# Performance work log

Hardware: AMD Instinct MI355X
Metric: run time of the kernel (lower is better)

## Reference

```python
import jax, jax.numpy as jnp
import numpy as np

WIN = 8
HEADS = 8
DOWN = 4
STRIDE = WIN // DOWN  # 2
LEVELS = len([i for i in range(8) if WIN / DOWN**i >= 1])  # 2
EPS = 1e-5


def circular_pad(x, pad_r, pad_b):
    # x: (N, H, W, C) -> (N, H+pad_b, W+pad_r, C), circular repeat like torch repeat+slice
    N, H, W, C = x.shape
    Hr = -(-(H + pad_b) // H)
    Wr = -(-(W + pad_r) // W)
    return jnp.tile(x, (1, Hr, Wr, 1))[:, :H + pad_b, :W + pad_r, :]


def pad_fit_win(x, ws):
    N, H, W, C = x.shape
    H_ = -(-H // ws) * ws
    W_ = -(-W // ws) * ws
    return circular_pad(x, W_ - W, H_ - H)


def window_partition(x, ws):
    N, H, W, C = x.shape
    x = x.reshape(N, H // ws, ws, W // ws, ws, C)
    return x.transpose(0, 1, 3, 2, 4, 5).reshape(-1, ws, ws, C)


def window_reverse(w, ws, H, W):
    B = w.shape[0] // ((H // ws) * (W // ws))
    x = w.reshape(B, H // ws, W // ws, ws, ws, -1)
    return x.transpose(0, 1, 3, 2, 4, 5).reshape(B, H, W, -1)


def layernorm(x, g, b):
    mu = jnp.mean(x, -1, keepdims=True)
    var = jnp.var(x, -1, keepdims=True)
    return (x - mu) * jax.lax.rsqrt(var + EPS) * g + b


def mha(q, k, v, wq, wk, wv, wf, bf):
    # q: (B, Lq, C); k, v: (B, Lk, C). Weights stored as (in, out); eval mode (no dropout).
    B, Lq, C = q.shape
    Lk = k.shape[1]
    dh = C // HEADS
    qh = (q @ wq).reshape(B, Lq, HEADS, dh)
    kh = (k @ wk).reshape(B, Lk, HEADS, dh)
    vh = (v @ wv).reshape(B, Lk, HEADS, dh)
    attn = jnp.einsum('bqhd,bkhd->bhqk', qh, kh) * (1.0 / dh ** 0.5)
    attn = jax.nn.softmax(attn, axis=-1)
    o = jnp.einsum('bhqk,bkhd->bqhd', attn, vh).reshape(B, Lq, C)
    return o @ wf + bf


def self_attention(x, wq, wk, wv, wf, bf):
    N, H, W, C = x.shape
    xp = pad_fit_win(x, WIN)
    _, H_, W_, _ = xp.shape
    xw = window_partition(xp, WIN).reshape(-1, WIN * WIN, C)
    res = mha(xw, xw, xw, wq, wk, wv, wf, bf)
    res = window_reverse(res.reshape(-1, WIN, WIN, C), WIN, H_, W_)
    return (xp + res)[:, :H, :W, :]


def cross_attention(q, kv, wq, wk, wv, wf, bf):
    # q: (N,qH,qW,C) non-overlapping windows; kv: (N,kH,kW,C) overlapping unfold windows
    N, qH, qW, C = q.shape
    _, kH, kW, _ = kv.shape
    qp = pad_fit_win(q, WIN)
    _, qH_, qW_, _ = qp.shape
    qw = window_partition(qp, WIN).reshape(-1, WIN * WIN, C)
    kH_ = (-(-kH // STRIDE) - 1) * STRIDE + WIN
    kW_ = (-(-kW // STRIDE) - 1) * STRIDE + WIN
    kvp = circular_pad(kv, kW_ - kW, kH_ - kH)
    nH = (kH_ - WIN) // STRIDE + 1
    nW = (kW_ - WIN) // STRIDE + 1
    ri = (jnp.arange(nH) * STRIDE)[:, None] + jnp.arange(WIN)
    ci = (jnp.arange(nW) * STRIDE)[:, None] + jnp.arange(WIN)
    patches = kvp[:, ri][:, :, :, ci]
    patches = patches.transpose(0, 1, 3, 2, 4, 5).reshape(-1, WIN * WIN, C)
    res = mha(qw, patches, patches, wq, wk, wv, wf, bf)
    res = window_reverse(res.reshape(-1, WIN, WIN, C), WIN, qH_, qW_)
    return (qp + res)[:, :qH, :qW, :]


def avgpool4(x):  # NHWC avg pool with kernel=stride=DOWN
    N, H, W, C = x.shape
    return x.reshape(N, H // DOWN, DOWN, W // DOWN, DOWN, C).mean((2, 4))


def setup_inputs() -> dict:
    key = jax.random.key(0)
    ks = jax.random.split(key, 12)
    D, DF = 256, 1024
    N, H, W = 8, 128, 128
    s = 0.02

    def w(k, shape):
        return jax.random.normal(k, shape, jnp.float32) * s

    return {
        'x': jax.random.normal(ks[0], (N, D, H, W), jnp.float32),
        'sa_wq': w(ks[1], (D, D)), 'sa_wk': w(ks[2], (D, D)), 'sa_wv': w(ks[3], (D, D)),
        'sa_wf': w(ks[4], (D, D)), 'sa_bf': jnp.zeros((D,), jnp.float32),
        'ca_wq': w(ks[5], (D, D)), 'ca_wk': w(ks[6], (D, D)), 'ca_wv': w(ks[7], (D, D)),
        'ca_wf': w(ks[8], (D, D)), 'ca_bf': jnp.zeros((D,), jnp.float32),
        'ln_self_g': jnp.ones((D,), jnp.float32), 'ln_self_b': jnp.zeros((D,), jnp.float32),
        'ln_cross_g': jnp.ones((D,), jnp.float32), 'ln_cross_b': jnp.zeros((D,), jnp.float32),
        'ffn_w1': w(ks[9], (D, DF)), 'ffn_b1': jnp.zeros((DF,), jnp.float32),
        'ffn_w2': w(ks[10], (DF, D)), 'ffn_b2': jnp.zeros((D,), jnp.float32),
        'ln_out_g': jnp.ones((D,), jnp.float32), 'ln_out_b': jnp.zeros((D,), jnp.float32),
    }


def reference(x, sa_wq, sa_wk, sa_wv, sa_wf, sa_bf,
              ca_wq, ca_wk, ca_wv, ca_wf, ca_bf,
              ln_self_g, ln_self_b, ln_cross_g, ln_cross_b,
              ffn_w1, ffn_b1, ffn_w2, ffn_b2, ln_out_g, ln_out_b):
    N, C, H, W = x.shape
    xh = x.transpose(0, 2, 3, 1)  # NHWC
    xh = pad_fit_win(xh, WIN)
    attn_list = []
    for idx in range(LEVELS):
        xa = self_attention(xh, sa_wq, sa_wk, sa_wv, sa_wf, sa_bf)
        xa = layernorm(xa, ln_self_g, ln_self_b)
        attn_list.append(xa)
        if idx < LEVELS - 1:
            xh = avgpool4(xa)
    kv = attn_list[-1]
    for idx in range(LEVELS - 1, 0, -1):
        q = cross_attention(attn_list[idx - 1], kv, ca_wq, ca_wk, ca_wv, ca_wf, ca_bf)
        q = layernorm(q, ln_cross_g, ln_cross_b)
        kv = q
    q = kv[:, :H, :W, :]
    res = jax.nn.relu(q @ ffn_w1 + ffn_b1) @ ffn_w2 + ffn_b2
    out = layernorm(q + res, ln_out_g, ln_out_b)
    return out.transpose(0, 3, 1, 2)
```

## Files before the change

### kernel.cpp

```cpp
#include <hip/hip_runtime.h>

typedef _Float16 h16;
typedef _Float16 f16x8 __attribute__((ext_vector_type(8)));
typedef _Float16 f16x4 __attribute__((ext_vector_type(4)));
typedef float f32x4 __attribute__((ext_vector_type(4)));

__device__ __forceinline__ float b2f(h16 v){ return (float)v; }
__device__ __forceinline__ h16 f2b(float v){ return (h16)v; }

#define CDIM 256
#define NHEADS 8
#define DH 32

__global__ __launch_bounds__(256) void k_wt_all(const float* __restrict__ s0, const float* __restrict__ s1,
                                                const float* __restrict__ s2, const float* __restrict__ s3,
                                                const float* __restrict__ s4, const float* __restrict__ s5,
                                                const float* __restrict__ s6, const float* __restrict__ s7,
                                                const float* __restrict__ s8, const float* __restrict__ s9,
                                                h16* __restrict__ wsc)
{
    __shared__ float T[32][33];
    int b = blockIdx.x;
    const float* src; h16* dst; int K, N, ti, tj;
    if (b < 512) {
        int w = b >> 6, rem = b & 63;
        ti = rem >> 3; tj = rem & 7; K = 256; N = 256;
        switch (w) {
            case 0: src = s0; break; case 1: src = s1; break;
            case 2: src = s2; break; case 3: src = s3; break;
            case 4: src = s4; break; case 5: src = s5; break;
            case 6: src = s6; break; default: src = s7; break;
        }
        dst = wsc + w * 65536;
    } else if (b < 768) {
        int rem = b - 512; ti = rem >> 5; tj = rem & 31; K = 256; N = 1024;
        src = s8; dst = wsc + 8 * 65536;
    } else {
        int rem = b - 768; ti = rem >> 3; tj = rem & 7; K = 1024; N = 256;
        src = s9; dst = wsc + 8 * 65536 + 262144;
    }
    int rr = threadIdx.x >> 5, c = threadIdx.x & 31;
    #pragma unroll
    for (int i = 0; i < 4; ++i) {
        int r = i * 8 + rr;
        T[r][c] = src[(long long)(ti * 32 + r) * N + tj * 32 + c];
    }
    __syncthreads();
    #pragma unroll
    for (int i = 0; i < 4; ++i) {
        int r = i * 8 + rr;
        dst[(long long)(tj * 32 + r) * K + ti * 32 + c] = f2b(T[c][r]);
    }
}

__global__ __launch_bounds__(256) void k_nchw2nhwc(const float* __restrict__ x, h16* __restrict__ o,
                                                   int Hh, int Ww)
{
    __shared__ float T[64][65];
    int bid = blockIdx.x;
    int cb = bid & 3; bid >>= 2;
    int nwb = Ww >> 6;
    int wb = bid % nwb; bid /= nwb;
    int h = bid % Hh;
    int n = bid / Hh;
    int lane = threadIdx.x & 63, grp = threadIdx.x >> 6;
    int w0 = wb << 6;
    long long HW = (long long)Hh * Ww;
    long long rbase = ((long long)(n * CDIM + cb * 64) * Hh + h) * Ww + w0;
    #pragma unroll
    for (int i = 0; i < 16; ++i) {
        int cl = grp * 16 + i;
        T[cl][lane] = x[rbase + (long long)cl * HW + lane];
    }
    __syncthreads();
    long long obase = (long long)(n * Hh + h) * Ww + w0;
    #pragma unroll
    for (int i = 0; i < 16; ++i) {
        int wl = grp * 16 + i;
        o[(obase + wl) * CDIM + cb * 64 + lane] = f2b(T[lane][wl]);
    }
}

__global__ __launch_bounds__(256) void k_gemm_mfma(const h16* __restrict__ A, const h16* __restrict__ Bt,
                                                   const float* __restrict__ bias, const h16* __restrict__ Cadd,
                                                   h16* __restrict__ C,
                                                   int N, int K, int ldA, int ldbt, int ldc,
                                                   long long ostride, int relu)
{
    __shared__ __align__(16) h16 As[128 * 64];
    __shared__ __align__(16) h16 Bs[128 * 64];
    const int tid = threadIdx.x;
    const int wave = tid >> 6, lane = tid & 63;
    const int l15 = lane & 15, g = lane >> 4;
    const int gx = gridDim.x;
    int L = blockIdx.y * gx + blockIdx.x;
    const int nwg = gx * gridDim.y;
    if ((nwg & 7) == 0) {
        const int cpx = nwg >> 3;
        L = (L & 7) * cpx + (L >> 3);
    }
    const int row0 = (L / gx) * 128, col0 = (L % gx) * 128;
    const int wm = (wave >> 1) * 64, wn = (wave & 1) * 64;

    f32x4 acc[4][4] = {};

    const int srow = wave * 32 + (lane >> 3);
    const int sch  = ((lane & 7) ^ (srow & 7)) * 8;
    const h16* ag = A  + (long long)(row0 + srow) * ldA  + sch;
    const h16* bg = Bt + (long long)(col0 + srow) * ldbt + sch;
    h16* as_base = As + (wave * 32) * 64;
    h16* bs_base = Bs + (wave * 32) * 64;

    for (int k0 = 0; k0 < K; k0 += 64) {
        #pragma unroll
        for (int i = 0; i < 4; ++i) {
            __builtin_amdgcn_global_load_lds(
                (const __attribute__((address_space(1))) void*)(ag + (long long)i * 8 * ldA),
                (__attribute__((address_space(3))) void*)(as_base + i * 8 * 64), 16, 0, 0);
            __builtin_amdgcn_global_load_lds(
                (const __attribute__((address_space(1))) void*)(bg + (long long)i * 8 * ldbt),
                (__attribute__((address_space(3))) void*)(bs_base + i * 8 * 64), 16, 0, 0);
        }
        ag += 64; bg += 64;
        __syncthreads();
        #pragma unroll
        for (int kk = 0; kk < 2; ++kk) {
            const int c = kk * 4 + g;
            const int slot = (c ^ (l15 & 7)) << 3;
            f16x8 af[4], bb[4];
            #pragma unroll
            for (int i = 0; i < 4; ++i) {
                af[i] = *(const f16x8*)(As + (wm + i * 16 + l15) * 64 + slot);
                bb[i] = *(const f16x8*)(Bs + (wn + i * 16 + l15) * 64 + slot);
            }
            #pragma unroll
            for (int i = 0; i < 4; ++i)
                #pragma unroll
                for (int j = 0; j < 4; ++j)
                    acc[i][j] = __builtin_amdgcn_mfma_f32_16x16x32_f16(af[i], bb[j], acc[i][j], 0, 0, 0);
        }
        __syncthreads();
    }

    const int cr = g * 4;
    #pragma unroll
    for (int j = 0; j < 4; ++j) {
        int col = col0 + wn + j * 16 + l15;
        int grp = col >> 8;
        long long cb = (long long)grp * ostride + (col & 255);
        float bv = bias ? bias[col] : 0.f;
        #pragma unroll
        for (int i = 0; i < 4; ++i) {
            #pragma unroll
            for (int r = 0; r < 4; ++r) {
                long long row = row0 + wm + i * 16 + cr + r;
                float v = acc[i][j][r] + bv;
                if (relu) v = fmaxf(v, 0.f);
                long long addr = cb + row * ldc;
                if (Cadd) v += b2f(Cadd[addr]);
                C[addr] = f2b(v);
            }
        }
    }
}

__global__ __launch_bounds__(512) void k_gemm_ln(const h16* __restrict__ A, const h16* __restrict__ Bt,
                                                 const float* __restrict__ bias, const h16* __restrict__ Cadd,
                                                 const h16* __restrict__ R,
                                                 const float* __restrict__ gw, const float* __restrict__ bw,
                                                 h16* __restrict__ O16, float* __restrict__ O32,
                                                 int K, int ldA, int ldbt, int HW, int mode)
{
    __shared__ __align__(16) h16 As[128 * 64];
    __shared__ __align__(16) h16 Bs[256 * 64];
    __shared__ float red[2][128][4];
    const int tid = threadIdx.x;
    const int wave = tid >> 6, lane = tid & 63;
    const int l15 = lane & 15, g = lane >> 4;
    const int row0 = blockIdx.x * 128;
    const int wm = (wave >> 2) * 64, wn = (wave & 3) * 64;

    f32x4 acc[4][4] = {};

    const int ar = wave * 16 + (lane >> 3);
    const int br = wave * 32 + (lane >> 3);
    const int ach = ((lane & 7) ^ (ar & 7)) * 8;
    const int bch = ((lane & 7) ^ (br & 7)) * 8;
    const h16* ag = A  + (long long)(row0 + ar) * ldA + ach;
    const h16* bg = Bt + (long long)br * ldbt + bch;
    h16* as_base = As + (wave * 16) * 64;
    h16* bs_base = Bs + (wave * 32) * 64;

    for (int k0 = 0; k0 < K; k0 += 64) {
        #pragma unroll
        for (int i = 0; i < 2; ++i)
            __builtin_amdgcn_global_load_lds(
                (const __attribute__((address_space(1))) void*)(ag + (long long)i * 8 * ldA),
                (__attribute__((address_space(3))) void*)(as_base + i * 8 * 64), 16, 0, 0);
        #pragma unroll
        for (int i = 0; i < 4; ++i)
            __builtin_amdgcn_global_load_lds(
                (const __attribute__((address_space(1))) void*)(bg + (long long)i * 8 * ldbt),
                (__attribute__((address_space(3))) void*)(bs_base + i * 8 * 64), 16, 0, 0);
        ag += 64; bg += 64;
        __syncthreads();
        #pragma unroll
        for (int kk = 0; kk < 2; ++kk) {
            const int c = kk * 4 + g;
            const int slot = (c ^ (l15 & 7)) << 3;
            f16x8 af[4], bb[4];
            #pragma unroll
            for (int i = 0; i < 4; ++i) {
                af[i] = *(const f16x8*)(As + (wm + i * 16 + l15) * 64 + slot);
                bb[i] = *(const f16x8*)(Bs + (wn + i * 16 + l15) * 64 + slot);
            }
            #pragma unroll
            for (int i = 0; i < 4; ++i)
                #pragma unroll
                for (int j = 0; j < 4; ++j)
                    acc[i][j] = __builtin_amdgcn_mfma_f32_16x16x32_f16(af[i], bb[j], acc[i][j], 0, 0, 0);
        }
        __syncthreads();
    }

    float sr[4][4] = {}, sr2[4][4] = {};
    #pragma unroll
    for (int j = 0; j < 4; ++j) {
        int col = wn + j * 16 + l15;
        float bv = bias ? bias[col] : 0.f;
        #pragma unroll
        for (int i = 0; i < 4; ++i) {
            #pragma unroll
            for (int r = 0; r < 4; ++r) {
                long long row = row0 + wm + i * 16 + g * 4 + r;
                float u = acc[i][j][r] + bv;
                if (Cadd) u += b2f(Cadd[row * CDIM + col]);
                u += b2f(R[row * CDIM + col]);
                acc[i][j][r] = u;
                sr[i][r] += u; sr2[i][r] += u * u;
            }
        }
    }
    #pragma unroll
    for (int i = 0; i < 4; ++i)
        #pragma unroll
        for (int r = 0; r < 4; ++r) {
            float s = sr[i][r], s2 = sr2[i][r];
            #pragma unroll
            for (int off = 1; off < 16; off <<= 1) { s += __shfl_xor(s, off); s2 += __shfl_xor(s2, off); }
            sr[i][r] = s; sr2[i][r] = s2;
        }
    if (l15 == 0) {
        #pragma unroll
        for (int i = 0; i < 4; ++i)
            #pragma unroll
            for (int r = 0; r < 4; ++r) {
                int lr = wm + i * 16 + g * 4 + r;
                red[0][lr][wave & 3] = sr[i][r];
                red[1][lr][wave & 3] = sr2[i][r];
            }
    }
    __syncthreads();
    float mu_[4][4], iv_[4][4];
    #pragma unroll
    for (int i = 0; i < 4; ++i)
        #pragma unroll
        for (int r = 0; r < 4; ++r) {
            int lr = wm + i * 16 + g * 4 + r;
            f32x4 p = *(const f32x4*)&red[0][lr][0];
            f32x4 q = *(const f32x4*)&red[1][lr][0];
            float ts  = p[0] + p[1] + p[2] + p[3];
            float ts2 = q[0] + q[1] + q[2] + q[3];
            float mu = ts * (1.f / 256.f);
            mu_[i][r] = mu;
            iv_[i][r] = rsqrtf(ts2 * (1.f / 256.f) - mu * mu + 1e-5f);
        }
    if (mode == 0) {
        #pragma unroll
        for (int j = 0; j < 4; ++j) {
            int col = wn + j * 16 + l15;
            float gc = gw[col], bc = bw[col];
            #pragma unroll
            for (int i = 0; i < 4; ++i)
                #pragma unroll
                for (int r = 0; r < 4; ++r) {
                    long long row = row0 + wm + i * 16 + g * 4 + r;
                    O16[row * CDIM + col] = f2b((acc[i][j][r] - mu_[i][r]) * iv_[i][r] * gc + bc);
                }
        }
    } else {
        #pragma unroll
        for (int j = 0; j < 4; ++j) {
            int col = wn + j * 16 + l15;
            float gc = gw[col], bc = bw[col];
            #pragma unroll
            for (int i = 0; i < 4; ++i) {
                int tok0 = row0 + wm + i * 16 + g * 4;
                int n = tok0 / HW, hw = tok0 - n * HW;
                f32x4 y;
                #pragma unroll
                for (int r = 0; r < 4; ++r)
                    y[r] = (acc[i][j][r] - mu_[i][r]) * iv_[i][r] * gc + bc;
                *(f32x4*)(O32 + (long long)(n * CDIM + col) * HW + hw) = y;
            }
        }
    }
}

__global__ __launch_bounds__(256) void k_attn_mfma(const h16* __restrict__ Q, const h16* __restrict__ Kp,
                                                   const h16* __restrict__ Vp, h16* __restrict__ O,
                                                   int Hh, int Ww, int cross)
{
    __shared__ __align__(16) h16 SpA[4][64 * 64];
    __shared__ __align__(16) h16 VtA[4][32 * 64];
    const int tid = threadIdx.x;
    const int wave = tid >> 6, lane = tid & 63;
    const int l15 = lane & 15, g = lane >> 4;
    h16* Sp = SpA[wave];
    h16* Vt = VtA[wave];

    const int win = blockIdx.x;
    int n, wi, wj;
    if (cross) { n = win >> 8; wi = (win >> 4) & 15; wj = win & 15; }
    else {
        int nw = Ww >> 3, nh = Hh >> 3;
        n = win / (nh * nw);
        int rem = win - n * (nh * nw);
        wi = rem / nw; wj = rem - (rem / nw) * nw;
    }
    auto qtok = [&](int t) {
        return cross ? (n * 128 + wi * 8 + (t >> 3)) * 128 + wj * 8 + (t & 7)
                     : (n * Hh + wi * 8 + (t >> 3)) * Ww + wj * 8 + (t & 7);
    };
    auto ktok = [&](int t) {
        return cross ? (n * 32 + ((wi * 2 + (t >> 3)) & 31)) * 32 + ((wj * 2 + (t & 7)) & 31)
                     : qtok(t);
    };
    const float scale = 0.17677669529663687f;

    int qt_frag[4], kt_frag[4];
    #pragma unroll
    for (int i = 0; i < 4; ++i) { qt_frag[i] = qtok(i * 16 + l15); kt_frag[i] = ktok(i * 16 + l15); }
    const int vtok = ktok(lane);
    int otok[4][4];
    #pragma unroll
    for (int qt = 0; qt < 4; ++qt)
        #pragma unroll
        for (int rr = 0; rr < 4; ++rr)
            otok[qt][rr] = qtok(qt * 16 + g * 4 + rr);

    #pragma unroll 1
    for (int hh = 0; hh < 2; ++hh) {
        const int h = wave * 2 + hh;
        const int hoff = h * 32;

        f16x8 vin[4];
        #pragma unroll
        for (int j = 0; j < 4; ++j)
            vin[j] = *(const f16x8*)(Vp + (long long)vtok * CDIM + hoff + j * 8);

        f16x8 kf[4], qf[4];
        #pragma unroll
        for (int i = 0; i < 4; ++i) {
            kf[i] = *(const f16x8*)(Kp + (long long)kt_frag[i] * CDIM + hoff + g * 8);
            qf[i] = *(const f16x8*)(Q  + (long long)qt_frag[i] * CDIM + hoff + g * 8);
        }

        #pragma unroll
        for (int j = 0; j < 4; ++j)
            #pragma unroll
            for (int e = 0; e < 8; ++e) {
                int d = j * 8 + e;
                Vt[(d * 64 + lane) ^ ((d & 7) << 3)] = vin[j][e];
            }

        f32x4 sT[4][4] = {};
        #pragma unroll
        for (int i = 0; i < 4; ++i)
            #pragma unroll
            for (int jq = 0; jq < 4; ++jq)
                sT[i][jq] = __builtin_amdgcn_mfma_f32_16x16x32_f16(kf[i], qf[jq], sT[i][jq], 0, 0, 0);

        #pragma unroll
        for (int jq = 0; jq < 4; ++jq) {
            float m = -1e30f;
            #pragma unroll
            for (int i = 0; i < 4; ++i)
                #pragma unroll
                for (int rr = 0; rr < 4; ++rr)
                    m = fmaxf(m, sT[i][jq][rr]);
            m = fmaxf(m, __shfl_xor(m, 16));
            m = fmaxf(m, __shfl_xor(m, 32));
            float p[16];
            float sum = 0.f;
            #pragma unroll
            for (int i = 0; i < 4; ++i)
                #pragma unroll
                for (int rr = 0; rr < 4; ++rr) {
                    float e = __expf((sT[i][jq][rr] - m) * scale);
                    p[i * 4 + rr] = e; sum += e;
                }
            sum += __shfl_xor(sum, 16);
            sum += __shfl_xor(sum, 32);
            float inv = 1.f / sum;
            int q = jq * 16 + l15;
            int rowbase = q * 64, swz = (q & 7) << 3;
            #pragma unroll
            for (int i = 0; i < 4; ++i) {
                f16x4 pk;
                pk[0] = (h16)(p[i * 4 + 0] * inv);
                pk[1] = (h16)(p[i * 4 + 1] * inv);
                pk[2] = (h16)(p[i * 4 + 2] * inv);
                pk[3] = (h16)(p[i * 4 + 3] * inv);
                *(f16x4*)(Sp + ((rowbase + i * 16 + g * 4) ^ swz)) = pk;
            }
        }
        asm volatile("s_waitcnt lgkmcnt(0)" ::: "memory");

        f32x4 o[4][2] = {};
        #pragma unroll
        for (int kb = 0; kb < 2; ++kb) {
            f16x8 vb[2];
            #pragma unroll
            for (int dt = 0; dt < 2; ++dt) {
                int d = dt * 16 + l15;
                vb[dt] = *(const f16x8*)(Vt + ((d * 64 + kb * 32 + g * 8) ^ ((d & 7) << 3)));
            }
            #pragma unroll
            for (int qt = 0; qt < 4; ++qt) {
                int q = qt * 16 + l15;
                f16x8 pa = *(const f16x8*)(Sp + ((q * 64 + kb * 32 + g * 8) ^ ((q & 7) << 3)));
                #pragma unroll
                for (int dt = 0; dt < 2; ++dt)
                    o[qt][dt] = __builtin_amdgcn_mfma_f32_16x16x32_f16(pa, vb[dt], o[qt][dt], 0, 0, 0);
            }
        }

        #pragma unroll
        for (int qt = 0; qt < 4; ++qt)
            #pragma unroll
            for (int rr = 0; rr < 4; ++rr) {
                long long tb = (long long)otok[qt][rr] * CDIM + hoff;
                #pragma unroll
                for (int dt = 0; dt < 2; ++dt)
                    O[tb + dt * 16 + l15] = f2b(o[qt][dt][rr]);
            }
        asm volatile("s_waitcnt lgkmcnt(0)" ::: "memory");
    }
}

__global__ __launch_bounds__(256) void k_ln_out(const h16* __restrict__ A, const h16* __restrict__ Bb,
                                                const float* __restrict__ g, const float* __restrict__ be,
                                                float* __restrict__ O, int HW)
{
    __shared__ float Y[32][257];
    int tid = threadIdx.x;
    int t = tid >> 5;
    int j = tid & 31;
    long long tok0 = (long long)blockIdx.x * 32;
    f32x4 g0 = *(const f32x4*)(g + j * 8),  g1 = *(const f32x4*)(g + j * 8 + 4);
    f32x4 e0 = *(const f32x4*)(be + j * 8), e1 = *(const f32x4*)(be + j * 8 + 4);
    #pragma unroll
    for (int pass = 0; pass < 4; ++pass) {
        int ta = pass * 8 + t;
        long long base = (tok0 + ta) * CDIM + j * 8;
        f16x8 a = *(const f16x8*)(A + base);
        f16x8 b = *(const f16x8*)(Bb + base);
        float v[8]; float s = 0.f, s2 = 0.f;
        #pragma unroll
        for (int e = 0; e < 8; ++e) { float vv = b2f(a[e]) + b2f(b[e]); v[e] = vv; s += vv; s2 += vv * vv; }
        #pragma unroll
        for (int off = 1; off < 32; off <<= 1) { s += __shfl_xor(s, off); s2 += __shfl_xor(s2, off); }
        float mu = s * (1.f / 256.f);
        float inv = rsqrtf(s2 * (1.f / 256.f) - mu * mu + 1e-5f);
        #pragma unroll
        for (int e = 0; e < 4; ++e) Y[ta][j * 8 + e]     = (v[e] - mu) * inv * g0[e] + e0[e];
        #pragma unroll
        for (int e = 0; e < 4; ++e) Y[ta][j * 8 + 4 + e] = (v[e + 4] - mu) * inv * g1[e] + e1[e];
    }
    __syncthreads();
    int n = (int)(tok0 / HW);
    int hw0 = (int)(tok0 - (long long)n * HW);
    int tt = tid & 31;
    int cw = tid >> 5;
    #pragma unroll
    for (int k = 0; k < 32; ++k) {
        int c = k * 8 + cw;
        O[((long long)(n * CDIM + c)) * HW + hw0 + tt] = Y[tt][c];
    }
}

__global__ __launch_bounds__(256) void k_pool(const h16* __restrict__ A, h16* __restrict__ P,
                                              int Hin, int Win)
{
    int tok = blockIdx.x, c = threadIdx.x;
    int Wo = Win >> 2, Ho = Hin >> 2;
    int n = tok / (Ho * Wo);
    int rem = tok - n * (Ho * Wo);
    int i = rem / Wo, j = rem - (rem / Wo) * Wo;
    float s = 0.f;
    #pragma unroll
    for (int di = 0; di < 4; ++di)
        #pragma unroll
        for (int dj = 0; dj < 4; ++dj)
            s += b2f(A[(((long long)n * Hin + i * 4 + di) * Win + j * 4 + dj) * CDIM + c]);
    P[(long long)tok * CDIM + c] = f2b(s * 0.0625f);
}

extern "C" void kernel_launch(void* const* d_in, const int* in_sizes, int n_in,
                              void* d_out, int out_size, void* d_ws, size_t ws_size,
                              hipStream_t stream)
{
    const float* x     = (const float*)d_in[0];
    const float* sa_wq = (const float*)d_in[1];
    const float* sa_wk = (const float*)d_in[2];
    const float* sa_wv = (const float*)d_in[3];
    const float* sa_wf = (const float*)d_in[4];
    const float* sa_bf = (const float*)d_in[5];
    const float* ca_wq = (const float*)d_in[6];
    const float* ca_wk = (const float*)d_in[7];
    const float* ca_wv = (const float*)d_in[8];
    const float* ca_wf = (const float*)d_in[9];
    const float* ca_bf = (const float*)d_in[10];
    const float* lns_g = (const float*)d_in[11];
    const float* lns_b = (const float*)d_in[12];
    const float* lnc_g = (const float*)d_in[13];
    const float* lnc_b = (const float*)d_in[14];
    const float* w1    = (const float*)d_in[15];
    const float* b1    = (const float*)d_in[16];
    const float* w2    = (const float*)d_in[17];
    const float* b2    = (const float*)d_in[18];
    const float* lno_g = (const float*)d_in[19];
    const float* lno_b = (const float*)d_in[20];
    float* out = (float*)d_out;

    const int TOK0 = 8 * 128 * 128;
    const int TOK1 = 8 * 32 * 32;
    const size_t S0  = (size_t)TOK0 * CDIM * sizeof(h16);
    const size_t SML = (size_t)TOK1 * CDIM * sizeof(h16);
    char* ws = (char*)d_ws;
    h16* W0 = (h16*)(ws);
    h16* W1 = (h16*)(ws + S0);
    h16* W2 = (h16*)(ws + 2 * S0);
    h16* W3 = (h16*)(ws + 3 * S0);
    h16* H  = W2;
    h16* P1 = (h16*)(ws + 0 * SML);
    h16* Q1 = (h16*)(ws + 1 * SML);
    h16* K1 = (h16*)(ws + 2 * SML);
    h16* V1 = (h16*)(ws + 3 * SML);
    h16* A1 = (h16*)(ws + 5 * SML);
    h16* Kc = (h16*)(ws + 6 * SML);
    h16* Vc = (h16*)(ws + 7 * SML);

    const size_t WSC_BYTES = (8 * 65536 + 262144 + 262144) * sizeof(h16);
    bool tailws = ws_size >= 4 * S0 + WSC_BYTES;
    h16* wsc = tailws ? (h16*)(ws + 4 * S0) : (h16*)d_out;
    h16* sa_wqT = wsc + 0 * 65536;
    h16* sa_wfT = wsc + 3 * 65536;
    h16* ca_wqT = wsc + 4 * 65536;
    h16* ca_wkT = wsc + 5 * 65536;
    h16* ca_wfT = wsc + 7 * 65536;
    h16* w1T    = wsc + 8 * 65536;
    h16* w2T    = wsc + 8 * 65536 + 262144;

    const long long OS0 = (long long)TOK0 * CDIM;
    const long long OS1 = (long long)TOK1 * CDIM;

    dim3 blk(256), blk2(512);

    k_wt_all<<<1024, blk, 0, stream>>>(sa_wq, sa_wk, sa_wv, sa_wf, ca_wq, ca_wk, ca_wv, ca_wf,
                                       w1, w2, wsc);

    k_nchw2nhwc<<<8 * 128 * 2 * 4, blk, 0, stream>>>(x, W0, 128, 128);
    k_gemm_mfma<<<dim3(6, TOK0 / 128), blk, 0, stream>>>(W0, sa_wqT, nullptr, nullptr, W1, 768, 256, 256, 256, 256, OS0, 0);
    k_attn_mfma<<<TOK0 / 64, blk, 0, stream>>>(W1, W2, W3, W1, 128, 128, 0);
    k_gemm_ln<<<TOK0 / 128, blk2, 0, stream>>>(W1, sa_wfT, sa_bf, nullptr, W0, lns_g, lns_b,
                                               W3, nullptr, 256, 256, 256, 16384, 0);

    k_pool<<<TOK1, blk, 0, stream>>>(W3, P1, 128, 128);
    k_gemm_mfma<<<dim3(6, TOK1 / 128), blk, 0, stream>>>(P1, sa_wqT, nullptr, nullptr, Q1, 768, 256, 256, 256, 256, OS1, 0);
    k_attn_mfma<<<TOK1 / 64, blk, 0, stream>>>(Q1, K1, V1, Q1, 32, 32, 0);
    k_gemm_ln<<<TOK1 / 128, blk2, 0, stream>>>(Q1, sa_wfT, sa_bf, nullptr, P1, lns_g, lns_b,
                                               A1, nullptr, 256, 256, 256, 1024, 0);

    k_gemm_mfma<<<dim3(2, TOK0 / 128), blk, 0, stream>>>(W3, ca_wqT, nullptr, nullptr, W1, 256, 256, 256, 256, 256, 0, 0);
    k_gemm_mfma<<<dim3(4, TOK1 / 128), blk, 0, stream>>>(A1, ca_wkT, nullptr, nullptr, Kc, 512, 256, 256, 256, 256, OS1, 0);
    k_attn_mfma<<<TOK0 / 64, blk, 0, stream>>>(W1, Kc, Vc, W1, 0, 0, 1);
    k_gemm_ln<<<TOK0 / 128, blk2, 0, stream>>>(W1, ca_wfT, ca_bf, nullptr, W3, lnc_g, lnc_b,
                                               W1, nullptr, 256, 256, 256, 16384, 0);

    k_gemm_mfma<<<dim3(4, TOK0 / 128), blk, 0, stream>>>(W1, w1T,             b1,       nullptr, H,  512, 256, 256, 256, 512, 256, 1);
    k_gemm_mfma<<<dim3(2, TOK0 / 128), blk, 0, stream>>>(H,  w2T,             b2,       nullptr, W0, 256, 512, 512, 1024, 256, 0, 0);
    k_gemm_mfma<<<dim3(4, TOK0 / 128), blk, 0, stream>>>(W1, w1T + 512 * 256, b1 + 512, nullptr, H,  512, 256, 256, 256, 512, 256, 1);
    if (tailws) {
        k_gemm_ln<<<TOK0 / 128, blk2, 0, stream>>>(H, w2T + 512, nullptr, W0, W1, lno_g, lno_b,
                                                   nullptr, out, 512, 512, 1024, 16384, 1);
    } else {
        k_gemm_mfma<<<dim3(2, TOK0 / 128), blk, 0, stream>>>(H, w2T + 512, nullptr, W0, W0, 256, 512, 512, 1024, 256, 0, 0);
        k_ln_out<<<TOK0 / 32, blk, 0, stream>>>(W1, W0, lno_g, lno_b, out, 16384);
    }
}
```

Baseline: 1.156 ms.

## Double-buffer LDS tiles in MFMA GEMM kernels to overlap loads with compute

Both GEMM kernels now use two LDS buffers per operand. The next K tile is issued with async global-to-LDS loads before the current tile is computed, and partial vmcnt waits replace the full __syncthreads. The goal is to hide global memory latency behind the MFMA work. The cost is twice the LDS use, which may lower occupancy, especially in the LN kernel with its 256-wide B tile. Ordering now relies on hand-set vmcnt counts, which must match the number of loads issued per stage.

```diff
diff --git a/kernel.cpp b/kernel.cpp
--- a/kernel.cpp
+++ b/kernel.cpp
@@ -87,8 +87,8 @@
                                                    int N, int K, int ldA, int ldbt, int ldc,
                                                    long long ostride, int relu)
 {
-    __shared__ __align__(16) h16 As[128 * 64];
-    __shared__ __align__(16) h16 Bs[128 * 64];
+    __shared__ __align__(16) h16 As[2 * 128 * 64];
+    __shared__ __align__(16) h16 Bs[2 * 128 * 64];
     const int tid = threadIdx.x;
     const int wave = tid >> 6, lane = tid & 63;
     const int l15 = lane & 15, g = lane >> 4;
@@ -111,18 +111,35 @@
     h16* as_base = As + (wave * 32) * 64;
     h16* bs_base = Bs + (wave * 32) * 64;
 
-    for (int k0 = 0; k0 < K; k0 += 64) {
+    const int NT = K >> 6;
+    auto stage = [&](int t, int buf) {
+        const h16* a = ag + (long long)t * 64;
+        const h16* b = bg + (long long)t * 64;
+        h16* ad = as_base + buf * (128 * 64);
+        h16* bd = bs_base + buf * (128 * 64);
         #pragma unroll
         for (int i = 0; i < 4; ++i) {
             __builtin_amdgcn_global_load_lds(
-                (const __attribute__((address_space(1))) void*)(ag + (long long)i * 8 * ldA),
-                (__attribute__((address_space(3))) void*)(as_base + i * 8 * 64), 16, 0, 0);
+                (const __attribute__((address_space(1))) void*)(a + (long long)i * 8 * ldA),
+                (__attribute__((address_space(3))) void*)(ad + i * 8 * 64), 16, 0, 0);
             __builtin_amdgcn_global_load_lds(
-                (const __attribute__((address_space(1))) void*)(bg + (long long)i * 8 * ldbt),
-                (__attribute__((address_space(3))) void*)(bs_base + i * 8 * 64), 16, 0, 0);
-        }
-        ag += 64; bg += 64;
-        __syncthreads();
+                (const __attribute__((address_space(1))) void*)(b + (long long)i * 8 * ldbt),
+                (__attribute__((address_space(3))) void*)(bd + i * 8 * 64), 16, 0, 0);
+        }
+    };
+
+    stage(0, 0);
+    int cur = 0;
+    for (int t = 0; t < NT; ++t) {
+        if (t + 1 < NT) {
+            stage(t + 1, cur ^ 1);
+            asm volatile("s_waitcnt vmcnt(8)" ::: "memory");
+        } else {
+            asm volatile("s_waitcnt vmcnt(0)" ::: "memory");
+        }
+        __builtin_amdgcn_s_barrier();
+        const h16* Ab = As + cur * (128 * 64);
+        const h16* Bb2 = Bs + cur * (128 * 64);
         #pragma unroll
         for (int kk = 0; kk < 2; ++kk) {
             const int c = kk * 4 + g;
@@ -130,8 +147,8 @@
             f16x8 af[4], bb[4];
             #pragma unroll
             for (int i = 0; i < 4; ++i) {
-                af[i] = *(const f16x8*)(As + (wm + i * 16 + l15) * 64 + slot);
-                bb[i] = *(const f16x8*)(Bs + (wn + i * 16 + l15) * 64 + slot);
+                af[i] = *(const f16x8*)(Ab + (wm + i * 16 + l15) * 64 + slot);
+                bb[i] = *(const f16x8*)(Bb2 + (wn + i * 16 + l15) * 64 + slot);
             }
             #pragma unroll
             for (int i = 0; i < 4; ++i)
@@ -139,10 +156,10 @@
                 for (int j = 0; j < 4; ++j)
                     acc[i][j] = __builtin_amdgcn_mfma_f32_16x16x32_f16(af[i], bb[j], acc[i][j], 0, 0, 0);
         }
-        __syncthreads();
-    }
-
-    const int cr = g * 4;
+        __builtin_amdgcn_s_barrier();
+        cur ^= 1;
+    }
+
     #pragma unroll
     for (int j = 0; j < 4; ++j) {
         int col = col0 + wn + j * 16 + l15;
@@ -153,7 +170,7 @@
         for (int i = 0; i < 4; ++i) {
             #pragma unroll
             for (int r = 0; r < 4; ++r) {
-                long long row = row0 + wm + i * 16 + cr + r;
+                long long row = row0 + wm + i * 16 + g * 4 + r;
                 float v = acc[i][j][r] + bv;
                 if (relu) v = fmaxf(v, 0.f);
                 long long addr = cb + row * ldc;
@@ -171,8 +188,8 @@
                                                  h16* __restrict__ O16, float* __restrict__ O32,
                                                  int K, int ldA, int ldbt, int HW, int mode)
 {
-    __shared__ __align__(16) h16 As[128 * 64];
-    __shared__ __align__(16) h16 Bs[256 * 64];
+    __shared__ __align__(16) h16 As[2 * 128 * 64];
+    __shared__ __align__(16) h16 Bs[2 * 256 * 64];
     __shared__ float red[2][128][4];
     const int tid = threadIdx.x;
     const int wave = tid >> 6, lane = tid & 63;
@@ -191,19 +208,36 @@
     h16* as_base = As + (wave * 16) * 64;
     h16* bs_base = Bs + (wave * 32) * 64;
 
-    for (int k0 = 0; k0 < K; k0 += 64) {
+    const int NT = K >> 6;
+    auto stage = [&](int t, int buf) {
+        const h16* a = ag + (long long)t * 64;
+        const h16* b = bg + (long long)t * 64;
+        h16* ad = as_base + buf * (128 * 64);
+        h16* bd = bs_base + buf * (256 * 64);
         #pragma unroll
         for (int i = 0; i < 2; ++i)
             __builtin_amdgcn_global_load_lds(
-                (const __attribute__((address_space(1))) void*)(ag + (long long)i * 8 * ldA),
-                (__attribute__((address_space(3))) void*)(as_base + i * 8 * 64), 16, 0, 0);
+                (const __attribute__((address_space(1))) void*)(a + (long long)i * 8 * ldA),
+                (__attribute__((address_space(3))) void*)(ad + i * 8 * 64), 16, 0, 0);
         #pragma unroll
         for (int i = 0; i < 4; ++i)
             __builtin_amdgcn_global_load_lds(
-                (const __attribute__((address_space(1))) void*)(bg + (long long)i * 8 * ldbt),
-                (__attribute__((address_space(3))) void*)(bs_base + i * 8 * 64), 16, 0, 0);
-        ag += 64; bg += 64;
-        __syncthreads();
+                (const __attribute__((address_space(1))) void*)(b + (long long)i * 8 * ldbt),
+                (__attribute__((address_space(3))) void*)(bd + i * 8 * 64), 16, 0, 0);
+    };
+
+    stage(0, 0);
+    int cur = 0;
+    for (int t = 0; t < NT; ++t) {
+        if (t + 1 < NT) {
+            stage(t + 1, cur ^ 1);
+            asm volatile("s_waitcnt vmcnt(6)" ::: "memory");
+        } else {
+            asm volatile("s_waitcnt vmcnt(0)" ::: "memory");
+        }
+        __builtin_amdgcn_s_barrier();
+        const h16* Ab = As + cur * (128 * 64);
+        const h16* Bb2 = Bs + cur * (256 * 64);
         #pragma unroll
         for (int kk = 0; kk < 2; ++kk) {
             const int c = kk * 4 + g;
@@ -211,8 +245,8 @@
             f16x8 af[4], bb[4];
             #pragma unroll
             for (int i = 0; i < 4; ++i) {
-                af[i] = *(const f16x8*)(As + (wm + i * 16 + l15) * 64 + slot);
-                bb[i] = *(const f16x8*)(Bs + (wn + i * 16 + l15) * 64 + slot);
+                af[i] = *(const f16x8*)(Ab + (wm + i * 16 + l15) * 64 + slot);
+                bb[i] = *(const f16x8*)(Bb2 + (wn + i * 16 + l15) * 64 + slot);
             }
             #pragma unroll
             for (int i = 0; i < 4; ++i)
@@ -220,7 +254,8 @@
                 for (int j = 0; j < 4; ++j)
                     acc[i][j] = __builtin_amdgcn_mfma_f32_16x16x32_f16(af[i], bb[j], acc[i][j], 0, 0, 0);
         }
-        __syncthreads();
+        __builtin_amdgcn_s_barrier();
+        cur ^= 1;
     }
 
     float sr[4][4] = {}, sr2[4][4] = {};
```

Result: faster. 1.128 ms (-2.4%).
